# Kernel tuning notes

Measured on AMD Instinct MI355X. Metric: run time of the kernel, lower is better.

## Reference

```python
import jax, jax.numpy as jnp
import numpy as np

B_SZ, L, H, P, V, OUT_LEN = 32, 4096, 512, 384, 32, 16
DT_MIN, DT_MAX = 0.001, 0.1


def setup_inputs() -> dict:
    key = jax.random.key(0)
    ks = jax.random.split(key, 12)
    tokens = jax.random.randint(ks[0], (B_SZ, L), 0, V, dtype=jnp.int32)
    embed = jax.random.normal(ks[1], (V, H), dtype=jnp.float32) * 0.02
    # S5 diagonal state: Lambda = Lambda_re + i*Lambda_im (stable: Re < 0)
    Lambda_re = -0.5 * jax.random.uniform(ks[2], (P,), dtype=jnp.float32) - 1e-3
    Lambda_im = jnp.pi * jnp.arange(P, dtype=jnp.float32)
    B_re = jax.random.normal(ks[3], (P, H), dtype=jnp.float32) / np.sqrt(H)
    B_im = jax.random.normal(ks[4], (P, H), dtype=jnp.float32) / np.sqrt(H)
    C_re = jax.random.normal(ks[5], (H, P), dtype=jnp.float32) / np.sqrt(P)
    C_im = jax.random.normal(ks[6], (H, P), dtype=jnp.float32) / np.sqrt(P)
    D = jax.random.normal(ks[7], (H,), dtype=jnp.float32)
    log_step = jax.random.uniform(
        ks[8], (P,), dtype=jnp.float32,
        minval=np.log(DT_MIN), maxval=np.log(DT_MAX))
    W1 = jax.random.normal(ks[9], (H, H), dtype=jnp.float32) / np.sqrt(H)
    b1 = jnp.zeros((H,), dtype=jnp.float32)
    W2 = jax.random.normal(ks[10], (H, V), dtype=jnp.float32) / np.sqrt(H)
    b2 = jnp.zeros((V,), dtype=jnp.float32)
    return dict(tokens=tokens, embed=embed, Lambda_re=Lambda_re,
                Lambda_im=Lambda_im, B_re=B_re, B_im=B_im, C_re=C_re,
                C_im=C_im, D=D, log_step=log_step, W1=W1, b1=b1, W2=W2, b2=b2)


def _s5_scan(Lbar, Bu_bar):
    # Lbar: (P,) complex; Bu_bar: (B,L,P) complex
    A = jnp.broadcast_to(Lbar, Bu_bar.shape)

    def comb(e1, e2):
        A1, b1 = e1
        A2, b2 = e2
        return A2 * A1, A2 * b1 + b2

    _, xs = jax.lax.associative_scan(comb, (A, Bu_bar), axis=1)
    return xs  # (B,L,P) hidden states


def reference(tokens, embed, Lambda_re, Lambda_im, B_re, B_im,
              C_re, C_im, D, log_step, W1, b1, W2, b2):
    u = embed[tokens]                              # (B,L,H) real
    Lam = Lambda_re + 1j * Lambda_im               # (P,)
    step = jnp.exp(log_step)                       # (P,)
    Lbar = jnp.exp(Lam * step)                     # ZOH: exp(Lambda*dt)
    Bc = B_re + 1j * B_im                          # (P,H)
    Cc = C_re + 1j * C_im                          # (H,P)
    Bu = jnp.einsum('blh,ph->blp', u, Bc)          # (B,L,P) complex
    Bu_bar = ((Lbar - 1.0) / Lam) * Bu             # ZOH input discretization
    xs = _s5_scan(Lbar, Bu_bar)                    # (B,L,P)
    # conj_sym=True -> 2 * Re(C x) + D u
    y = 2.0 * jnp.einsum('blp,hp->blh', xs, Cc).real + u * D
    y = y[:, -OUT_LEN:, :]                         # (B,16,H)
    h = jax.nn.relu(y @ W1 + b1)
    return h @ W2 + b2                             # (B,16,V)
```

## Files before the change

### kernel.cpp

```cpp
#include <hip/hip_runtime.h>

#define B_SZ 32
#define L 4096
#define H 512
#define P 384
#define V 32
#define OUT_LEN 16
#define NC 32
#define CHUNK 127
#define T0 4064

#define OFF_DBL   0
#define OFF_LBARF 4608
#define OFF_M     5376
#define OFF_CT    29952
#define OFF_PART  423168
#define OFF_YT    1209600
#define OFF_HP    1471744

__global__ __launch_bounds__(256) void k_prep(
    const int* __restrict__ tokens, const float* __restrict__ embed,
    const float* __restrict__ Lre, const float* __restrict__ Lim,
    const float* __restrict__ Bre, const float* __restrict__ Bim,
    const float* __restrict__ Cre, const float* __restrict__ Cim,
    const float* __restrict__ log_step, float* __restrict__ ws)
{
    __shared__ float sre[32][33], sim[32][33];
    int bx = blockIdx.x, tid = threadIdx.x;
    if (bx < 2) {
        int p = bx * 256 + tid;
        if (p < P) {
            double dstep = exp((double)log_step[p]);
            double are = (double)Lre[p] * dstep, aim = (double)Lim[p] * dstep;
            double mag = exp(are);
            double lbr = mag * cos(aim), lbi = mag * sin(aim);
            double wmag = exp((double)CHUNK * are);
            double wang = (double)CHUNK * aim;
            double wr = wmag * cos(wang), wi = wmag * sin(wang);
            double lre = (double)Lre[p], lim = (double)Lim[p];
            double nr = lbr - 1.0, ni = lbi;
            double den = lre * lre + lim * lim;
            double cr = (nr * lre + ni * lim) / den, ci = (ni * lre - nr * lim) / den;
            double* d = (double*)ws + p * 6;
            d[0] = lbr; d[1] = lbi; d[2] = wr; d[3] = wi; d[4] = cr; d[5] = ci;
            ws[OFF_LBARF + 2 * p]     = (float)lbr;
            ws[OFF_LBARF + 2 * p + 1] = (float)lbi;
        }
    } else if (bx < 194) {
        int bxx = bx - 2;
        int tp = bxx >> 4, th = bxx & 15;
        int col = tid & 31, r0 = tid >> 5;
        #pragma unroll
        for (int it = 0; it < 4; ++it) {
            int row = r0 + 8 * it;
            int h = th * 32 + row, p = tp * 32 + col;
            sre[col][row] = Cre[h * P + p];
            sim[col][row] = Cim[h * P + p];
        }
        __syncthreads();
        #pragma unroll
        for (int it = 0; it < 4; ++it) {
            int pl = r0 + 8 * it;
            int p = tp * 32 + pl, h = th * 32 + col;
            ws[OFF_CT + (2 * p) * H + h]     = sre[pl][col];
            ws[OFF_CT + (2 * p + 1) * H + h] = sim[pl][col];
        }
    }
    {
        int w = bx * 4 + (tid >> 6);
        if (w < 1536) {
            int v0 = (w & 3) * 8, p = w >> 2;
            int lane = tid & 63;
            const float4* brp = (const float4*)(Bre + p * H);
            const float4* bip = (const float4*)(Bim + p * H);
            float4 br0 = brp[lane], br1 = brp[lane + 64];
            float4 bi0 = bip[lane], bi1 = bip[lane + 64];
            #pragma unroll
            for (int vv = 0; vv < 8; ++vv) {
                const float4* evp = (const float4*)(embed + (v0 + vv) * H);
                float4 e0 = evp[lane], e1 = evp[lane + 64];
                float dr = br0.x * e0.x;
                dr = fmaf(br0.y, e0.y, dr); dr = fmaf(br0.z, e0.z, dr);
                dr = fmaf(br0.w, e0.w, dr); dr = fmaf(br1.x, e1.x, dr);
                dr = fmaf(br1.y, e1.y, dr); dr = fmaf(br1.z, e1.z, dr);
                dr = fmaf(br1.w, e1.w, dr);
                float di = bi0.x * e0.x;
                di = fmaf(bi0.y, e0.y, di); di = fmaf(bi0.z, e0.z, di);
                di = fmaf(bi0.w, e0.w, di); di = fmaf(bi1.x, e1.x, di);
                di = fmaf(bi1.y, e1.y, di); di = fmaf(bi1.z, e1.z, di);
                di = fmaf(bi1.w, e1.w, di);
                #pragma unroll
                for (int off = 32; off; off >>= 1) {
                    dr += __shfl_down(dr, off);
                    di += __shfl_down(di, off);
                }
                if (lane == 0) {
                    ws[OFF_M + ((v0 + vv) * P + p) * 2]     = dr;
                    ws[OFF_M + ((v0 + vv) * P + p) * 2 + 1] = di;
                }
            }
        }
    }
}

__global__ __launch_bounds__(256) void k_scan(
    const int* __restrict__ tokens, const float* __restrict__ ws,
    float* __restrict__ part)
{
    __shared__ float2 sM[V * 192];
    int bx = blockIdx.x, tid = threadIdx.x;
    int b = bx >> 4;
    int rem = bx & 15;
    int ph = rem & 1;
    int c0 = (rem >> 1) * 4;
    const float2* Mg = (const float2*)(ws + OFF_M);
    for (int f = tid; f < V * 192; f += 256) {
        int v = f / 192, i = f - v * 192;
        sM[f] = Mg[v * P + ph * 192 + i];
    }
    __syncthreads();
    if (tid < 192) {
        int p = ph * 192 + tid;
        float Lr = ws[OFF_LBARF + 2 * p], Li = ws[OFF_LBARF + 2 * p + 1];
        const int* tk0 = tokens + b * L + (c0 + 0) * CHUNK;
        const int* tk1 = tokens + b * L + (c0 + 1) * CHUNK;
        const int* tk2 = tokens + b * L + (c0 + 2) * CHUNK;
        const int* tk3 = tokens + b * L + (c0 + 3) * CHUNK;
        float ar0 = 0, ai0 = 0, ar1 = 0, ai1 = 0;
        float ar2 = 0, ai2 = 0, ar3 = 0, ai3 = 0;
        for (int i = 0; i < CHUNK; ++i) {
            int t0 = tk0[i], t1 = tk1[i], t2 = tk2[i], t3 = tk3[i];
            float2 m0 = sM[t0 * 192 + tid];
            float2 m1 = sM[t1 * 192 + tid];
            float2 m2 = sM[t2 * 192 + tid];
            float2 m3 = sM[t3 * 192 + tid];
            float n;
            n = fmaf(Lr, ar0, fmaf(-Li, ai0, m0.x));
            ai0 = fmaf(Lr, ai0, fmaf(Li, ar0, m0.y)); ar0 = n;
            n = fmaf(Lr, ar1, fmaf(-Li, ai1, m1.x));
            ai1 = fmaf(Lr, ai1, fmaf(Li, ar1, m1.y)); ar1 = n;
            n = fmaf(Lr, ar2, fmaf(-Li, ai2, m2.x));
            ai2 = fmaf(Lr, ai2, fmaf(Li, ar2, m2.y)); ar2 = n;
            n = fmaf(Lr, ar3, fmaf(-Li, ai3, m3.x));
            ai3 = fmaf(Lr, ai3, fmaf(Li, ar3, m3.y)); ar3 = n;
        }
        float* pt = part;
        pt[((b * NC + c0 + 0) * P + p) * 2]     = ar0;
        pt[((b * NC + c0 + 0) * P + p) * 2 + 1] = ai0;
        pt[((b * NC + c0 + 1) * P + p) * 2]     = ar1;
        pt[((b * NC + c0 + 1) * P + p) * 2 + 1] = ai1;
        pt[((b * NC + c0 + 2) * P + p) * 2]     = ar2;
        pt[((b * NC + c0 + 2) * P + p) * 2 + 1] = ai2;
        pt[((b * NC + c0 + 3) * P + p) * 2]     = ar3;
        pt[((b * NC + c0 + 3) * P + p) * 2 + 1] = ai3;
    }
}

__global__ __launch_bounds__(256) void k_y(
    const int* __restrict__ tokens, const float* __restrict__ embed,
    const float* __restrict__ D, float* __restrict__ ws)
{
    __shared__ float sxs[P * 16];
    __shared__ float sred[4 * 64 * 9];
    int bx = blockIdx.x, tid = threadIdx.x;
    int b = bx >> 4, x = bx & 15;
    int lh = x & 1, hq = x >> 1;
    #pragma unroll
    for (int pass = 0; pass < 2; ++pass) {
        int p = tid + pass * 256;
        if (p < P) {
            const double* d = (const double*)ws + p * 6;
            double lbr = d[0], lbi = d[1], wr = d[2], wi = d[3];
            double cr = d[4], ci = d[5];
            double zr = 0.0, zi = 0.0;
            const float* pp = ws + OFF_PART + (b * NC * P + p) * 2;
            #pragma unroll 8
            for (int c = 0; c < NC; ++c) {
                double pr = (double)pp[c * P * 2], pi = (double)pp[c * P * 2 + 1];
                double tr = wr * zr - wi * zi + pr;
                double ti = wr * zi + wi * zr + pi;
                zr = tr; zi = ti;
            }
            const float* M0 = ws + OFF_M;
            const int* tk = tokens + b * L + T0;
            #pragma unroll 8
            for (int j = 0; j < 32; ++j) {
                int t = tk[j];
                double mr = (double)M0[(t * P + p) * 2];
                double mi = (double)M0[(t * P + p) * 2 + 1];
                double tr = lbr * zr - lbi * zi + mr;
                double ti = lbr * zi + lbi * zr + mi;
                zr = tr; zi = ti;
                int jj = j - 16;
                if (jj >= 0 && (jj >> 3) == lh) {
                    int jl = jj & 7;
                    sxs[p * 16 + 2 * jl]     = (float)(cr * zr - ci * zi);
                    sxs[p * 16 + 2 * jl + 1] = (float)(cr * zi + ci * zr);
                }
            }
        }
    }
    __syncthreads();
    int hl = tid & 63, pg = tid >> 6;
    int h = hq * 64 + hl;
    const float* ct = ws + OFF_CT;
    float acc[8];
    #pragma unroll
    for (int i = 0; i < 8; ++i) acc[i] = 0.f;
    int p0 = pg * 96;
    #pragma unroll 2
    for (int q = 0; q < 96; ++q) {
        int p = p0 + q;
        float cre = ct[(2 * p) * H + h];
        float cim = ct[(2 * p + 1) * H + h];
        const float4* xv = (const float4*)(sxs + p * 16);
        float4 x0 = xv[0], x1 = xv[1], x2 = xv[2], x3 = xv[3];
        acc[0] = fmaf(cre, x0.x, fmaf(-cim, x0.y, acc[0]));
        acc[1] = fmaf(cre, x0.z, fmaf(-cim, x0.w, acc[1]));
        acc[2] = fmaf(cre, x1.x, fmaf(-cim, x1.y, acc[2]));
        acc[3] = fmaf(cre, x1.z, fmaf(-cim, x1.w, acc[3]));
        acc[4] = fmaf(cre, x2.x, fmaf(-cim, x2.y, acc[4]));
        acc[5] = fmaf(cre, x2.z, fmaf(-cim, x2.w, acc[5]));
        acc[6] = fmaf(cre, x3.x, fmaf(-cim, x3.y, acc[6]));
        acc[7] = fmaf(cre, x3.z, fmaf(-cim, x3.w, acc[7]));
    }
    #pragma unroll
    for (int i = 0; i < 8; ++i)
        sred[(pg * 64 + hl) * 9 + i] = acc[i];
    __syncthreads();
    #pragma unroll
    for (int oo = 0; oo < 2; ++oo) {
        int o = tid + 256 * oo;
        int ohl = o & 63, oi = o >> 6;
        float s = sred[ohl * 9 + oi] + sred[(64 + ohl) * 9 + oi]
                + sred[(128 + ohl) * 9 + oi] + sred[(192 + ohl) * 9 + oi];
        int l = lh * 8 + oi;
        int t = tokens[b * L + (L - OUT_LEN) + l];
        int hh = hq * 64 + ohl;
        ws[OFF_YT + (b * OUT_LEN + l) * H + hh] =
            2.f * s + embed[t * H + hh] * D[hh];
    }
}

__global__ __launch_bounds__(256) void k_fc1(
    const float* __restrict__ W1, const float* __restrict__ ws,
    float* __restrict__ hp)
{
    __shared__ float ys[128 * 8];
    int bx = blockIdx.x, tid = threadIdx.x;
    int rg = bx >> 3, jh = (bx >> 2) & 1, kc = bx & 3;
    int j = jh * 256 + tid;
    int r0 = rg * 8, k0 = kc * 128;
    const float* yt = ws + OFF_YT;
    int kk = tid & 127, rr = tid >> 7;
    #pragma unroll
    for (int it = 0; it < 4; ++it)
        ys[kk * 8 + rr + 2 * it] = yt[(r0 + rr + 2 * it) * H + k0 + kk];
    __syncthreads();
    const float* wp = W1 + k0 * H + j;
    float wreg[8];
    #pragma unroll
    for (int u = 0; u < 8; ++u) wreg[u] = wp[u * H];
    float acc[8] = {0, 0, 0, 0, 0, 0, 0, 0};
    for (int kb = 0; kb < 128; kb += 8) {
        float cur[8];
        #pragma unroll
        for (int u = 0; u < 8; ++u) cur[u] = wreg[u];
        if (kb + 8 < 128) {
            #pragma unroll
            for (int u = 0; u < 8; ++u) wreg[u] = wp[(kb + 8 + u) * H];
        }
        #pragma unroll
        for (int u = 0; u < 8; ++u) {
            const float4* y0 = (const float4*)(ys + (kb + u) * 8);
            float4 p0 = y0[0], p1 = y0[1];
            float a = cur[u];
            acc[0] = fmaf(p0.x, a, acc[0]);
            acc[1] = fmaf(p0.y, a, acc[1]);
            acc[2] = fmaf(p0.z, a, acc[2]);
            acc[3] = fmaf(p0.w, a, acc[3]);
            acc[4] = fmaf(p1.x, a, acc[4]);
            acc[5] = fmaf(p1.y, a, acc[5]);
            acc[6] = fmaf(p1.z, a, acc[6]);
            acc[7] = fmaf(p1.w, a, acc[7]);
        }
    }
    #pragma unroll
    for (int i = 0; i < 8; ++i)
        hp[(kc * 512 + r0 + i) * H + j] = acc[i];
}

__global__ __launch_bounds__(256) void k_fc2(
    const float* __restrict__ b1, const float* __restrict__ W2,
    const float* __restrict__ b2, const float* __restrict__ hp,
    float* __restrict__ out)
{
    __shared__ float sh[512];
    __shared__ float red[8 * 32];
    int r = blockIdx.x, tid = threadIdx.x;
    #pragma unroll
    for (int half = 0; half < 2; ++half) {
        int j = half * 256 + tid;
        float s = b1[j] + hp[r * H + j] + hp[(512 + r) * H + j]
                        + hp[(1024 + r) * H + j] + hp[(1536 + r) * H + j];
        sh[j] = fmaxf(s, 0.f);
    }
    __syncthreads();
    int seg = tid >> 5, o = tid & 31;
    const float* w2 = W2 + seg * 64 * V + o;
    const float* hv = sh + seg * 64;
    float a0 = 0.f, a1 = 0.f, a2 = 0.f, a3 = 0.f;
    #pragma unroll
    for (int q = 0; q < 16; ++q) {
        a0 = fmaf(hv[q],      w2[q * V],        a0);
        a1 = fmaf(hv[16 + q], w2[(16 + q) * V], a1);
        a2 = fmaf(hv[32 + q], w2[(32 + q) * V], a2);
        a3 = fmaf(hv[48 + q], w2[(48 + q) * V], a3);
    }
    red[seg * 32 + o] = (a0 + a1) + (a2 + a3);
    __syncthreads();
    if (tid < 32) {
        float s = b2[tid];
        #pragma unroll
        for (int ss = 0; ss < 8; ++ss) s += red[ss * 32 + tid];
        out[r * V + tid] = s;
    }
}

extern "C" void kernel_launch(void* const* d_in, const int* in_sizes, int n_in,
                              void* d_out, int out_size, void* d_ws, size_t ws_size,
                              hipStream_t stream)
{
    const int*   tokens = (const int*)d_in[0];
    const float* embed  = (const float*)d_in[1];
    const float* Lre    = (const float*)d_in[2];
    const float* Lim    = (const float*)d_in[3];
    const float* Bre    = (const float*)d_in[4];
    const float* Bim    = (const float*)d_in[5];
    const float* Cre    = (const float*)d_in[6];
    const float* Cim    = (const float*)d_in[7];
    const float* D      = (const float*)d_in[8];
    const float* lstep  = (const float*)d_in[9];
    const float* W1     = (const float*)d_in[10];
    const float* b1     = (const float*)d_in[11];
    const float* W2     = (const float*)d_in[12];
    const float* b2     = (const float*)d_in[13];
    float* out = (float*)d_out;
    float* ws  = (float*)d_ws;

    k_prep<<<384, 256, 0, stream>>>(tokens, embed, Lre, Lim, Bre, Bim,
                                    Cre, Cim, lstep, ws);
    k_scan<<<512, 256, 0, stream>>>(tokens, ws, ws + OFF_PART);
    k_y   <<<512, 256, 0, stream>>>(tokens, embed, D, ws);
    k_fc1 <<<512, 256, 0, stream>>>(W1, ws, ws + OFF_HP);
    k_fc2 <<<512, 256, 0, stream>>>(b1, W2, b2, ws + OFF_HP, out);
}
```

Measured before the change: 155.0 us.

## Split scan into more chunks and pre-scale partials by precomputed chunk powers

```diff
diff --git a/kernel.cpp b/kernel.cpp
--- a/kernel.cpp
+++ b/kernel.cpp
@@ -6,17 +6,18 @@
 #define P 384
 #define V 32
 #define OUT_LEN 16
-#define NC 32
-#define CHUNK 127
-#define T0 4064
+#define NC 48
+#define CHUNK 85
+#define T0 4080
 
 #define OFF_DBL   0
 #define OFF_LBARF 4608
-#define OFF_M     5376
-#define OFF_CT    29952
-#define OFF_PART  423168
-#define OFF_YT    1209600
-#define OFF_HP    1471744
+#define OFF_WPOW  5376
+#define OFF_M     79104
+#define OFF_CT    103680
+#define OFF_PART  496896
+#define OFF_YT    1676544
+#define OFF_HP    1938688
 
 __global__ __launch_bounds__(256) void k_prep(
     const int* __restrict__ tokens, const float* __restrict__ embed,
@@ -45,6 +46,15 @@
             d[0] = lbr; d[1] = lbi; d[2] = wr; d[3] = wi; d[4] = cr; d[5] = ci;
             ws[OFF_LBARF + 2 * p]     = (float)lbr;
             ws[OFF_LBARF + 2 * p + 1] = (float)lbi;
+            double* wpow = (double*)(ws + OFF_WPOW);
+            double awr = 1.0, awi = 0.0;
+            for (int c = NC - 1; c >= 0; --c) {
+                wpow[(c * P + p) * 2]     = awr;
+                wpow[(c * P + p) * 2 + 1] = awi;
+                double t = awr * wr - awi * wi;
+                awi = awr * wi + awi * wr;
+                awr = t;
+            }
         }
     } else if (bx < 194) {
         int bxx = bx - 2;
@@ -108,9 +118,7 @@
     float* __restrict__ part)
 {
     __shared__ float2 sM[V * 192];
-    int bx = blockIdx.x, tid = threadIdx.x;
-    int b = bx >> 4;
-    int rem = bx & 15;
+    int rem = blockIdx.x, b = blockIdx.y, tid = threadIdx.x;
     int ph = rem & 1;
     int c0 = (rem >> 1) * 4;
     const float2* Mg = (const float2*)(ws + OFF_M);
@@ -144,15 +152,19 @@
             n = fmaf(Lr, ar3, fmaf(-Li, ai3, m3.x));
             ai3 = fmaf(Lr, ai3, fmaf(Li, ar3, m3.y)); ar3 = n;
         }
+        const double* wpow = (const double*)(ws + OFF_WPOW);
         float* pt = part;
-        pt[((b * NC + c0 + 0) * P + p) * 2]     = ar0;
-        pt[((b * NC + c0 + 0) * P + p) * 2 + 1] = ai0;
-        pt[((b * NC + c0 + 1) * P + p) * 2]     = ar1;
-        pt[((b * NC + c0 + 1) * P + p) * 2 + 1] = ai1;
-        pt[((b * NC + c0 + 2) * P + p) * 2]     = ar2;
-        pt[((b * NC + c0 + 2) * P + p) * 2 + 1] = ai2;
-        pt[((b * NC + c0 + 3) * P + p) * 2]     = ar3;
-        pt[((b * NC + c0 + 3) * P + p) * 2 + 1] = ai3;
+        #pragma unroll
+        for (int k = 0; k < 4; ++k) {
+            double wr = wpow[((c0 + k) * P + p) * 2];
+            double wi = wpow[((c0 + k) * P + p) * 2 + 1];
+            double ar = (k == 0) ? ar0 : (k == 1) ? ar1 : (k == 2) ? ar2 : ar3;
+            double ai = (k == 0) ? ai0 : (k == 1) ? ai1 : (k == 2) ? ai2 : ai3;
+            double sr = wr * ar - wi * ai;
+            double si = wr * ai + wi * ar;
+            pt[((b * NC + c0 + k) * P + p) * 2]     = (float)sr;
+            pt[((b * NC + c0 + k) * P + p) * 2 + 1] = (float)si;
+        }
     }
 }
 
@@ -170,30 +182,35 @@
         int p = tid + pass * 256;
         if (p < P) {
             const double* d = (const double*)ws + p * 6;
-            double lbr = d[0], lbi = d[1], wr = d[2], wi = d[3];
-            double cr = d[4], ci = d[5];
-            double zr = 0.0, zi = 0.0;
+            double lbr = d[0], lbi = d[1], cr = d[4], ci = d[5];
             const float* pp = ws + OFF_PART + (b * NC * P + p) * 2;
-            #pragma unroll 8
-            for (int c = 0; c < NC; ++c) {
-                double pr = (double)pp[c * P * 2], pi = (double)pp[c * P * 2 + 1];
-                double tr = wr * zr - wi * zi + pr;
-                double ti = wr * zi + wi * zr + pi;
-                zr = tr; zi = ti;
+            double s0r = 0, s0i = 0, s1r = 0, s1i = 0;
+            double s2r = 0, s2i = 0, s3r = 0, s3i = 0;
+            #pragma unroll
+            for (int c = 0; c < NC; c += 4) {
+                s0r += (double)pp[(c + 0) * P * 2];
+                s0i += (double)pp[(c + 0) * P * 2 + 1];
+                s1r += (double)pp[(c + 1) * P * 2];
+                s1i += (double)pp[(c + 1) * P * 2 + 1];
+                s2r += (double)pp[(c + 2) * P * 2];
+                s2i += (double)pp[(c + 2) * P * 2 + 1];
+                s3r += (double)pp[(c + 3) * P * 2];
+                s3i += (double)pp[(c + 3) * P * 2 + 1];
             }
+            double zr = (s0r + s1r) + (s2r + s3r);
+            double zi = (s0i + s1i) + (s2i + s3i);
             const float* M0 = ws + OFF_M;
             const int* tk = tokens + b * L + T0;
-            #pragma unroll 8
-            for (int j = 0; j < 32; ++j) {
+            #pragma unroll
+            for (int j = 0; j < OUT_LEN; ++j) {
                 int t = tk[j];
                 double mr = (double)M0[(t * P + p) * 2];
                 double mi = (double)M0[(t * P + p) * 2 + 1];
                 double tr = lbr * zr - lbi * zi + mr;
                 double ti = lbr * zi + lbi * zr + mi;
                 zr = tr; zi = ti;
-                int jj = j - 16;
-                if (jj >= 0 && (jj >> 3) == lh) {
-                    int jl = jj & 7;
+                if ((j >> 3) == lh) {
+                    int jl = j & 7;
                     sxs[p * 16 + 2 * jl]     = (float)(cr * zr - ci * zi);
                     sxs[p * 16 + 2 * jl + 1] = (float)(cr * zi + ci * zr);
                 }
@@ -235,7 +252,7 @@
         float s = sred[ohl * 9 + oi] + sred[(64 + ohl) * 9 + oi]
                 + sred[(128 + ohl) * 9 + oi] + sred[(192 + ohl) * 9 + oi];
         int l = lh * 8 + oi;
-        int t = tokens[b * L + (L - OUT_LEN) + l];
+        int t = tokens[b * L + T0 + l];
         int hh = hq * 64 + ohl;
         ws[OFF_YT + (b * OUT_LEN + l) * H + hh] =
             2.f * s + embed[t * H + hh] * D[hh];
@@ -350,7 +367,7 @@
 
     k_prep<<<384, 256, 0, stream>>>(tokens, embed, Lre, Lim, Bre, Bim,
                                     Cre, Cim, lstep, ws);
-    k_scan<<<512, 256, 0, stream>>>(tokens, ws, ws + OFF_PART);
+    k_scan<<<dim3(24, 32), 256, 0, stream>>>(tokens, ws, ws + OFF_PART);
     k_y   <<<512, 256, 0, stream>>>(tokens, embed, D, ws);
     k_fc1 <<<512, 256, 0, stream>>>(W1, ws, ws + OFF_HP);
     k_fc2 <<<512, 256, 0, stream>>>(b1, W2, b2, ws + OFF_HP, out);
```

After: 148.0 us. -4.5%, faster.
